# Optimization experiments

Measured on AMD Instinct MI355X. Metric: run time of the kernel, lower is better.

The kernel has to match this reference:

```python
import jax, jax.numpy as jnp
import numpy as np
import math

PRE_D = 2048   # pre_d_model (scaled from 8192)
D = 4096       # d_model (scaled from 16384)
N = 64         # d_state (scaled from 128)
K = 4          # d_conv
EXP = 2
L = 128        # sequence_length
DI1 = EXP * PRE_D
DI2 = EXP * D
DTR1 = math.ceil(PRE_D / 16)
DTR2 = math.ceil(D / 16)


def _sinusoid(max_len, d):
    pe = np.zeros((max_len, d), np.float32)
    pos = np.arange(max_len, dtype=np.float32)[:, None]
    div = np.exp(np.arange(0, d, 2, dtype=np.float32) * (-math.log(10000.0) / d))
    pe[:, 0::2] = np.sin(pos * div)
    pe[:, 1::2] = np.cos(pos * div)
    return jnp.asarray(pe)


def _mamba_params(key, d_in, d_out, di, dtr, n, k):
    ks = jax.random.split(key, 6)
    s = 0.02
    dt = jnp.exp(jax.random.uniform(ks[4], (di,)) * (math.log(0.1) - math.log(1e-3)) + math.log(1e-3))
    return dict(
        in_proj=jax.random.normal(ks[0], (2 * di, d_in)) * s,
        conv_w=jax.random.normal(ks[1], (di, k)) * s,
        conv_b=jnp.zeros((di,)),
        x_proj=jax.random.normal(ks[2], (dtr + 2 * n, di)) * s,
        dt_w=jax.random.normal(ks[3], (di, dtr)) * s,
        dt_b=jnp.log(jnp.expm1(dt)),  # softplus^-1 of dt init
        A_log=jnp.log(jnp.tile(jnp.arange(1, n + 1, dtype=jnp.float32), (di, 1))),
        D=jnp.ones((di,)),
        out_proj=jax.random.normal(ks[5], (d_out, di)) * s,
    )


def setup_inputs() -> dict:
    key = jax.random.key(0)
    k1, k2, k3, k4 = jax.random.split(key, 4)
    inp = {
        'pe': _sinusoid(L, PRE_D),                              # (L, PRE_D)
        'to_cond_w': jax.random.normal(k3, (PRE_D, 1)) * 0.02,  # Linear(1 -> PRE_D)
        'to_cond_b': jnp.zeros((PRE_D,)),
        'condition': jax.random.normal(k4, (1,)),
        'batch': 1,
    }
    for pref, p in (('m1_', _mamba_params(k1, PRE_D, PRE_D, DI1, DTR1, N, K)),
                    ('m2_', _mamba_params(k2, PRE_D, D, DI2, DTR2, N, K))):
        for name, v in p.items():
            inp[pref + name] = v
    return inp


def _silu(x):
    return x * jax.nn.sigmoid(x)


def _mamba(x, in_w, cw, cb, xp_w, dt_w, dt_b, A_log, Dp, out_w, dtr, n):
    # x: (B, L, d_in)
    xz = x @ in_w.T                     # (B, L, 2*di)
    xr, z = jnp.split(xz, 2, axis=-1)
    kk = cw.shape[1]
    Lx = xr.shape[1]
    xpad = jnp.pad(xr, ((0, 0), (kk - 1, 0), (0, 0)))  # causal pad
    conv = sum(cw[:, i] * xpad[:, i:i + Lx, :] for i in range(kk)) + cb
    xr = _silu(conv)
    dbc = xr @ xp_w.T                   # (B, L, dtr + 2n)
    dt = dbc[..., :dtr]
    Bm = dbc[..., dtr:dtr + n]
    Cm = dbc[..., dtr + n:]
    dt = jax.nn.softplus(dt @ dt_w.T + dt_b)           # (B, L, di)
    A = -jnp.exp(A_log)                                 # (di, n)
    dA = jnp.exp(jnp.einsum('bld,dn->bldn', dt, A))
    dBx = jnp.einsum('bld,bln,bld->bldn', dt, Bm, xr)

    def comb(c1, c2):
        a1, b1 = c1
        a2, b2 = c2
        return a2 * a1, a2 * b1 + b2

    _, h = jax.lax.associative_scan(comb, (dA, dBx), axis=1)  # (B, L, di, n)
    y = jnp.einsum('bldn,bln->bld', h, Cm) + xr * Dp
    y = y * _silu(z)
    return y @ out_w.T


def reference(pe, to_cond_w, to_cond_b, condition,
              m1_in_proj, m1_conv_w, m1_conv_b, m1_x_proj, m1_dt_w, m1_dt_b, m1_A_log, m1_D, m1_out_proj,
              m2_in_proj, m2_conv_w, m2_conv_b, m2_x_proj, m2_dt_w, m2_dt_b, m2_A_log, m2_D, m2_out_proj,
              batch):
    cond = condition.reshape(-1, 1, 1)
    c = jnp.einsum('bli,oi->blo', cond, to_cond_w) + to_cond_b   # (Bc,1,PRE_D)
    x = jnp.tile(pe[None], (batch, 1, 1)) + c                    # (B, L, PRE_D)
    x = _mamba(x, m1_in_proj, m1_conv_w, m1_conv_b, m1_x_proj, m1_dt_w, m1_dt_b,
               m1_A_log, m1_D, m1_out_proj, DTR1, N)
    x = _mamba(x, m2_in_proj, m2_conv_w, m2_conv_b, m2_x_proj, m2_dt_w, m2_dt_b,
               m2_A_log, m2_D, m2_out_proj, DTR2, N)
    return x
```

## Files before the change

### kernel.cpp

```cpp
#include <hip/hip_runtime.h>
#include <hip/hip_bf16.h>
#include <math.h>


typedef __attribute__((ext_vector_type(8))) short short8_t;
typedef __attribute__((ext_vector_type(4))) float f32x4;

__device__ __forceinline__ float sigmoidf_(float x) {
  return 1.0f / (1.0f + __expf(-x));
}
__device__ __forceinline__ float softplusf_(float x) {
  return fmaxf(x, 0.0f) + log1pf(expf(-fabsf(x)));
}
__device__ __forceinline__ void splitbf(float f, ushort& h, ushort& lo) {
  __hip_bfloat16 hb = __float2bfloat16(f);
  h = *reinterpret_cast<ushort*>(&hb);
  float hf = __bfloat162float(hb);
  __hip_bfloat16 lb = __float2bfloat16(f - hf);
  lo = *reinterpret_cast<ushort*>(&lb);
}
__device__ __forceinline__ size_t poff(int l, int d) {
  return (size_t)(d >> 5) * 8192 + (size_t)((d >> 3) & 3) * 1024 +
         (size_t)l * 8 + (d & 7);
}

__global__ __launch_bounds__(256) void k_prep(const float* __restrict__ pe,
                                              const float* __restrict__ cw,
                                              const float* __restrict__ cb,
                                              const float* __restrict__ cond,
                                              ushort* __restrict__ xp) {
  int i = blockIdx.x * 256 + threadIdx.x;
  int d = i & 2047;
  int l = i >> 11;
  float v = pe[i] + cond[0] * cw[d] + cb[d];
  ushort h, lo;
  splitbf(v, h, lo);
  size_t o = poff(l, d);
  xp[o] = h;
  xp[o + 4096] = lo;
}

#define KW 128
__global__ __launch_bounds__(256, 2) void k_gemmW(const ushort* __restrict__ Ap,
                                                  const float* __restrict__ W, int ldw,
                                                  float* __restrict__ P,
                                                  int N, int Ks) {
  __shared__ ushort Ws[2][2][16][66][8];

  const int n0   = blockIdx.x * 64;
  const int s    = blockIdx.z;
  const int kbeg = s * Ks;
  const int t    = threadIdx.x;
  const int l    = t & 63;
  const int w    = t >> 6;
  const int wm   = w >> 1;
  const int wn   = w & 1;
  const int lr   = l & 15;
  const int lg   = l >> 4;

  f32x4 acc[4][2];
#pragma unroll
  for (int mi = 0; mi < 4; ++mi)
#pragma unroll
    for (int ni = 0; ni < 2; ++ni) acc[mi][ni] = (f32x4)(0.0f);

  const int nIter = Ks / KW;
  const int j0    = (blockIdx.x * 3 + s) & (nIter - 1);

  const float* pWg = W + (size_t)(n0 + 16 * w) * ldw + kbeg + 2 * l;
  const int skb = l >> 2;
  const int se  = 2 * (l & 3);
  const ushort* pA0 = Ap + (size_t)(kbeg >> 5) * 8192;
  const int arow = 64 * wm + lr;
  const int brow = 32 * wn + lr;

#pragma unroll
  for (int i = 0; i < 16; ++i) {
    float2 v = *(const float2*)(pWg + (size_t)i * ldw + (size_t)j0 * KW);
    ushort h0, lo0, h1, lo1;
    splitbf(v.x, h0, lo0);
    splitbf(v.y, h1, lo1);
    ushort2 hh; hh.x = h0; hh.y = h1;
    ushort2 ll; ll.x = lo0; ll.y = lo1;
    *(ushort2*)&Ws[0][0][skb][16 * w + i][se] = hh;
    *(ushort2*)&Ws[0][1][skb][16 * w + i][se] = ll;
  }
  __syncthreads();

  for (int jj = 0; jj < nIter; ++jj) {
    const int cur = (j0 + jj) & (nIter - 1);
    const int bi  = jj & 1;
    const bool more = (jj + 1 < nIter);

    short8_t ah[4][4], al[4][4];
#pragma unroll
    for (int c = 0; c < 4; ++c) {
      const ushort* pAj = pA0 + (size_t)(cur * 4 + c) * 8192;
#pragma unroll
      for (int mi = 0; mi < 4; ++mi) {
        const size_t fo = (size_t)lg * 1024 + (size_t)(arow + 16 * mi) * 8;
        ah[c][mi] = *(const short8_t*)(pAj + fo);
        al[c][mi] = *(const short8_t*)(pAj + 4096 + fo);
      }
    }
    float2 wv[16];
    if (more) {
      const size_t ko = (size_t)((j0 + jj + 1) & (nIter - 1)) * KW;
#pragma unroll
      for (int i = 0; i < 16; ++i)
        wv[i] = *(const float2*)(pWg + (size_t)i * ldw + ko);
    }
#pragma unroll
    for (int c = 0; c < 4; ++c) {
      short8_t bh[2], bl[2];
#pragma unroll
      for (int ni = 0; ni < 2; ++ni) {
        bh[ni] = *(const short8_t*)&Ws[bi][0][c * 4 + lg][brow + 16 * ni][0];
        bl[ni] = *(const short8_t*)&Ws[bi][1][c * 4 + lg][brow + 16 * ni][0];
      }
#pragma unroll
      for (int mi = 0; mi < 4; ++mi)
#pragma unroll
        for (int ni = 0; ni < 2; ++ni) {
          acc[mi][ni] = __builtin_amdgcn_mfma_f32_16x16x32_bf16(ah[c][mi], bh[ni], acc[mi][ni], 0, 0, 0);
          acc[mi][ni] = __builtin_amdgcn_mfma_f32_16x16x32_bf16(al[c][mi], bh[ni], acc[mi][ni], 0, 0, 0);
          acc[mi][ni] = __builtin_amdgcn_mfma_f32_16x16x32_bf16(ah[c][mi], bl[ni], acc[mi][ni], 0, 0, 0);
        }
    }
    if (more) {
#pragma unroll
      for (int i = 0; i < 16; ++i) {
        ushort h0, lo0, h1, lo1;
        splitbf(wv[i].x, h0, lo0);
        splitbf(wv[i].y, h1, lo1);
        ushort2 hh; hh.x = h0; hh.y = h1;
        ushort2 ll; ll.x = lo0; ll.y = lo1;
        *(ushort2*)&Ws[bi ^ 1][0][skb][16 * w + i][se] = hh;
        *(ushort2*)&Ws[bi ^ 1][1][skb][16 * w + i][se] = ll;
      }
    }
    __syncthreads();
  }

  float* Pd = P + (size_t)s * 128 * N + n0 + 32 * wn;
#pragma unroll
  for (int mi = 0; mi < 4; ++mi)
#pragma unroll
    for (int ni = 0; ni < 2; ++ni) {
#pragma unroll
      for (int jj = 0; jj < 4; ++jj) {
        const int m = 64 * wm + 16 * mi + 4 * lg + jj;
        Pd[(size_t)m * N + 16 * ni + lr] = acc[mi][ni][jj];
      }
    }
}

#define KSTEP 32
__global__ __launch_bounds__(256, 2) void k_gemm(const ushort* __restrict__ Ap,
                                                 const float* __restrict__ W, int ldw,
                                                 float* __restrict__ P,
                                                 int N, int Ks) {
  __shared__ ushort Ws[2][2][4][128][8];

  const int n0   = blockIdx.x * 128;
  const int s    = blockIdx.z;
  const int kbeg = s * Ks;
  const int t    = threadIdx.x;
  const int l    = t & 63;
  const int w    = t >> 6;
  const int wm   = w >> 1;
  const int wn   = w & 1;
  const int lr   = l & 15;
  const int lg   = l >> 4;

  f32x4 acc[4][4];
#pragma unroll
  for (int mi = 0; mi < 4; ++mi)
#pragma unroll
    for (int ni = 0; ni < 4; ++ni) acc[mi][ni] = (f32x4)(0.0f);

  const int srow = t >> 3;
  const int sk16 = t & 7;
  const int skb  = sk16 >> 1;
  const int se0  = (sk16 & 1) * 4;
  const float* pWg = W + (size_t)(n0 + srow) * ldw + kbeg + sk16 * 4;

  const ushort* pAc = Ap + (size_t)(kbeg >> 5) * 8192;
  const int arow = 64 * wm + lr;
  const int brow = 64 * wn + lr;

  const int nIter = Ks / KSTEP;
  float4 wv[4];

#pragma unroll
  for (int r = 0; r < 4; ++r)
    wv[r] = *(const float4*)(pWg + (size_t)(r * 32) * ldw);
#pragma unroll
  for (int r = 0; r < 4; ++r) {
    ushort4 h4, l4;
    splitbf(wv[r].x, h4.x, l4.x); splitbf(wv[r].y, h4.y, l4.y);
    splitbf(wv[r].z, h4.z, l4.z); splitbf(wv[r].w, h4.w, l4.w);
    *(ushort4*)&Ws[0][0][skb][srow + 32 * r][se0] = h4;
    *(ushort4*)&Ws[0][1][skb][srow + 32 * r][se0] = l4;
  }
  __syncthreads();

  for (int j = 0; j < nIter; ++j) {
    const int bi = j & 1;
    const bool more = (j + 1 < nIter);

    const ushort* pAj = pAc + (size_t)j * 8192;
    short8_t ah[4], al[4];
#pragma unroll
    for (int mi = 0; mi < 4; ++mi) {
      const size_t fo = (size_t)lg * 1024 + (size_t)(arow + 16 * mi) * 8;
      ah[mi] = *(const short8_t*)(pAj + fo);
      al[mi] = *(const short8_t*)(pAj + 4096 + fo);
    }
    if (more) {
      const size_t ko = (size_t)(j + 1) * KSTEP;
#pragma unroll
      for (int r = 0; r < 4; ++r)
        wv[r] = *(const float4*)(pWg + ko + (size_t)(r * 32) * ldw);
    }
    short8_t bh[4], bl[4];
#pragma unroll
    for (int ni = 0; ni < 4; ++ni) {
      bh[ni] = *(const short8_t*)&Ws[bi][0][lg][brow + 16 * ni][0];
      bl[ni] = *(const short8_t*)&Ws[bi][1][lg][brow + 16 * ni][0];
    }
#pragma unroll
    for (int mi = 0; mi < 4; ++mi)
#pragma unroll
      for (int ni = 0; ni < 4; ++ni) {
        acc[mi][ni] = __builtin_amdgcn_mfma_f32_16x16x32_bf16(ah[mi], bh[ni], acc[mi][ni], 0, 0, 0);
        acc[mi][ni] = __builtin_amdgcn_mfma_f32_16x16x32_bf16(al[mi], bh[ni], acc[mi][ni], 0, 0, 0);
        acc[mi][ni] = __builtin_amdgcn_mfma_f32_16x16x32_bf16(ah[mi], bl[ni], acc[mi][ni], 0, 0, 0);
      }
    if (more) {
#pragma unroll
      for (int r = 0; r < 4; ++r) {
        ushort4 h4, l4;
        splitbf(wv[r].x, h4.x, l4.x); splitbf(wv[r].y, h4.y, l4.y);
        splitbf(wv[r].z, h4.z, l4.z); splitbf(wv[r].w, h4.w, l4.w);
        *(ushort4*)&Ws[bi ^ 1][0][skb][srow + 32 * r][se0] = h4;
        *(ushort4*)&Ws[bi ^ 1][1][skb][srow + 32 * r][se0] = l4;
      }
    }
    __syncthreads();
  }

  float* Pd = P + (size_t)s * 128 * N + n0 + 64 * wn;
#pragma unroll
  for (int mi = 0; mi < 4; ++mi)
#pragma unroll
    for (int ni = 0; ni < 4; ++ni) {
#pragma unroll
      for (int jj = 0; jj < 4; ++jj) {
        const int m = 64 * wm + 16 * mi + 4 * lg + jj;
        Pd[(size_t)m * N + 16 * ni + lr] = acc[mi][ni][jj];
      }
    }
}

__global__ __launch_bounds__(256) void k_reduce(const float* __restrict__ P,
                                                float* __restrict__ Y,
                                                ushort* __restrict__ Yp,
                                                int MN, int N, int S, int ep,
                                                const float* __restrict__ bias) {
  int i = (blockIdx.x * 256 + threadIdx.x) * 4;
  if (i >= MN) return;
  float4 v = *(const float4*)&P[i];
  for (int s = 1; s < S; ++s) {
    float4 p = *(const float4*)&P[(size_t)s * MN + i];
    v.x += p.x; v.y += p.y; v.z += p.z; v.w += p.w;
  }
  int n = i % N;
  int l = i / N;
  if (ep & 1) {
    const float4 b = *(const float4*)&bias[n];
    v.x = softplusf_(v.x + b.x);
    v.y = softplusf_(v.y + b.y);
    v.z = softplusf_(v.z + b.z);
    v.w = softplusf_(v.w + b.w);
  }
  if (ep & 4) *(float4*)&Y[i] = v;
  if (ep & 2) {
    ushort4 h4, l4;
    splitbf(v.x, h4.x, l4.x);
    splitbf(v.y, h4.y, l4.y);
    splitbf(v.z, h4.z, l4.z);
    splitbf(v.w, h4.w, l4.w);
    size_t o = poff(l, n);
    *(ushort4*)&Yp[o] = h4;
    *(ushort4*)&Yp[o + 4096] = l4;
  }
}

__global__ __launch_bounds__(256) void k_reduceA(const float* __restrict__ P,
                                                 float* __restrict__ Y, int MN) {
  int g = blockIdx.y;
  int i = (blockIdx.x * 256 + threadIdx.x) * 4;
  if (i >= MN) return;
  const float* Pp = P + (size_t)g * 8 * MN;
  float4 v = *(const float4*)&Pp[i];
  for (int s = 1; s < 8; ++s) {
    float4 p = *(const float4*)&Pp[(size_t)s * MN + i];
    v.x += p.x; v.y += p.y; v.z += p.z; v.w += p.w;
  }
  *(float4*)&Y[(size_t)g * MN + i] = v;
}

__global__ __launch_bounds__(256) void k_conv_silu(const float* __restrict__ xz,
                                                   const float* __restrict__ cw,
                                                   const float* __restrict__ cb,
                                                   float* __restrict__ xc,
                                                   ushort* __restrict__ xcp,
                                                   int DI, int lg2DI) {
  int i = blockIdx.x * 256 + threadIdx.x;
  int l = i >> lg2DI;
  int d = i & (DI - 1);
  const float4 w = *(const float4*)&cw[d * 4];
  const float* xr = xz + d;
  int ld = 2 * DI;
  float s = cb[d];
  s += w.w * xr[l * ld];
  if (l >= 1) s += w.z * xr[(l - 1) * ld];
  if (l >= 2) s += w.y * xr[(l - 2) * ld];
  if (l >= 3) s += w.x * xr[(l - 3) * ld];
  float v = s * sigmoidf_(s);
  xc[i] = v;
  ushort h, lo;
  splitbf(v, h, lo);
  size_t o = poff(l, d);
  xcp[o] = h;
  xcp[o + 4096] = lo;
}

__global__ __launch_bounds__(256) void k_scan(const float* __restrict__ dt,
                                              const float* __restrict__ xc,
                                              const float* __restrict__ dbc,
                                              const float* __restrict__ A_log,
                                              const float* __restrict__ Dp,
                                              float* __restrict__ y,
                                              int DI, int DTR) {
  __shared__ float cs[4][32][65];
  const int wid = threadIdx.x >> 6;
  const int n   = threadIdx.x & 63;
  const int d   = blockIdx.x * 4 + wid;
  const int du  = __builtin_amdgcn_readfirstlane(d);
  const float A  = -__expf(A_log[(size_t)du * 64 + n]);
  const float Dd = Dp[du];
  const int ldbc = DTR + 128;
  const float* Bp = dbc + DTR + n;
  const float* Cp = dbc + DTR + 64 + n;
  float h = 0.0f;
  for (int l0 = 0; l0 < 128; l0 += 32) {
#pragma unroll 8
    for (int l = l0; l < l0 + 32; ++l) {
      float dtv = dt[(size_t)l * DI + du];
      float xcv = xc[(size_t)l * DI + du];
      float dA  = __expf(dtv * A);
      float bx  = dtv * xcv;
      h = fmaf(dA, h, bx * Bp[(size_t)l * ldbc]);
      cs[wid][l - l0][n] = h * Cp[(size_t)l * ldbc];
    }
    __syncthreads();
    const int r = n & 31, hf = n >> 5;
    float ssum = 0.0f;
#pragma unroll
    for (int j = 0; j < 32; ++j) ssum += cs[wid][r][hf * 32 + j];
    ssum += __shfl_xor(ssum, 32, 64);
    if (n < 32) {
      int ll = l0 + r;
      float xcv = xc[(size_t)ll * DI + du];
      y[(size_t)ll * DI + du] = ssum + xcv * Dd;
    }
    __syncthreads();
  }
}

__global__ __launch_bounds__(256) void k_gate(const float* __restrict__ yb,
                                              const float* __restrict__ xz,
                                              ushort* __restrict__ yp,
                                              int DI, int lg2DI) {
  int i = blockIdx.x * 256 + threadIdx.x;
  int l = i >> lg2DI;
  int d = i & (DI - 1);
  float z = xz[((size_t)l << (lg2DI + 1)) + DI + d];
  float v = yb[i] * (z * sigmoidf_(z));
  ushort h, lo;
  splitbf(v, h, lo);
  size_t o = poff(l, d);
  yp[o] = h;
  yp[o + 4096] = lo;
}

struct GemmCtx {
  float* part;
  float* part2;
  long long cap;
};

static inline void reduce_stage(float* dstF, ushort* dstP, int N, int S, int ep,
                                const float* bias, const GemmCtx& cx,
                                hipStream_t stream) {
  const int MN = 128 * N;
  const int rb = (MN / 4 + 255) / 256;
  if (S <= 16) {
    k_reduce<<<rb, 256, 0, stream>>>(cx.part, dstF, dstP, MN, N, S, ep, bias);
  } else {
    k_reduceA<<<dim3(rb, S / 8), 256, 0, stream>>>(cx.part, cx.part2, MN);
    k_reduce<<<rb, 256, 0, stream>>>(cx.part2, dstF, dstP, MN, N, S / 8, ep, bias);
  }
}

static inline void gemmS(const ushort* Ap, const float* W, int ldw,
                         float* dstF, ushort* dstP,
                         int N, int K, int Sdes, int ep,
                         const float* bias, const GemmCtx& cx, hipStream_t stream) {
  int S = Sdes;
  if (S > K / KSTEP) S = K / KSTEP;
  if (S < 1) S = 1;
  while (S > 1 && (long long)S * 128 * N > cx.cap) S >>= 1;
  const int Ks = K / S;
  const bool direct = (S == 1 && ep == 4);
  dim3 g(N / 128, 1, S);
  k_gemm<<<g, 256, 0, stream>>>(Ap, W, ldw, direct ? dstF : cx.part, N, Ks);
  if (!direct) reduce_stage(dstF, dstP, N, S, ep, bias, cx, stream);
}

static inline void gemmW(const ushort* Ap, const float* W, int ldw,
                         float* dstF, ushort* dstP,
                         int N, int K, int Sdes, int ep,
                         const float* bias, const GemmCtx& cx, hipStream_t stream) {
  int S = Sdes;
  if (S > K / KW) S = K / KW;
  if (S < 1) S = 1;
  while (S > 1 && (long long)S * 128 * N > cx.cap) S >>= 1;
  const int Ks = K / S;
  const bool direct = (S == 1 && ep == 4);
  dim3 g(N / 64, 1, S);
  k_gemmW<<<g, 256, 0, stream>>>(Ap, W, ldw, direct ? dstF : cx.part, N, Ks);
  if (!direct) reduce_stage(dstF, dstP, N, S, ep, bias, cx, stream);
}

extern "C" void kernel_launch(void* const* d_in, const int* in_sizes, int n_in,
                              void* d_out, int out_size, void* d_ws, size_t ws_size,
                              hipStream_t stream) {
  const float* pe        = (const float*)d_in[0];
  const float* to_cond_w = (const float*)d_in[1];
  const float* to_cond_b = (const float*)d_in[2];
  const float* condition = (const float*)d_in[3];
  const int o = (in_sizes[4] == 1) ? 5 : 4;
  const float* m1_in_proj  = (const float*)d_in[o + 0];
  const float* m1_conv_w   = (const float*)d_in[o + 1];
  const float* m1_conv_b   = (const float*)d_in[o + 2];
  const float* m1_x_proj   = (const float*)d_in[o + 3];
  const float* m1_dt_w     = (const float*)d_in[o + 4];
  const float* m1_dt_b     = (const float*)d_in[o + 5];
  const float* m1_A_log    = (const float*)d_in[o + 6];
  const float* m1_D        = (const float*)d_in[o + 7];
  const float* m1_out_proj = (const float*)d_in[o + 8];
  const float* m2_in_proj  = (const float*)d_in[o + 9];
  const float* m2_conv_w   = (const float*)d_in[o + 10];
  const float* m2_conv_b   = (const float*)d_in[o + 11];
  const float* m2_x_proj   = (const float*)d_in[o + 12];
  const float* m2_dt_w     = (const float*)d_in[o + 13];
  const float* m2_dt_b     = (const float*)d_in[o + 14];
  const float* m2_A_log    = (const float*)d_in[o + 15];
  const float* m2_D        = (const float*)d_in[o + 16];
  const float* m2_out_proj = (const float*)d_in[o + 17];

  float* ws = (float*)d_ws;
  float*  xz   = ws;
  float*  xc   = ws + 2097152;
  float*  dbc  = ws + 3145728;
  float*  dtb  = ws + 3194880;
  float*  yb   = ws + 4243456;
  ushort* x0p  = (ushort*)(ws + 5292032);
  ushort* xcp  = (ushort*)(ws + 5554176);
  ushort* dbcp = (ushort*)(ws + 6602752);
  ushort* ybp  = (ushort*)(ws + 6651904);
  ushort* midp = (ushort*)(ws + 7700480);
  float*  part2 = ws + 7962624;
  float*  part  = ws + 8749056;

  GemmCtx cx;
  cx.part = part;
  cx.part2 = part2;
  cx.cap = (long long)(ws_size / 4) - 8749056;
  if (cx.cap < 0) cx.cap = 0;

  k_prep<<<1024, 256, 0, stream>>>(pe, to_cond_w, to_cond_b, condition, x0p);

  gemmW(x0p, m1_in_proj, 2048, xz, nullptr, 8192, 2048, 4, 4, nullptr, cx, stream);
  k_conv_silu<<<(128 * 4096) / 256, 256, 0, stream>>>(xz, m1_conv_w, m1_conv_b,
                                                      xc, xcp, 4096, 12);
  gemmS(xcp, m1_x_proj, 4096, dbc, dbcp, 256, 4096, 128, 6, nullptr, cx, stream);
  gemmS(dbcp, m1_dt_w, 128, dtb, nullptr, 4096, 128, 4, 5, m1_dt_b, cx, stream);
  k_scan<<<1024, 256, 0, stream>>>(dtb, xc, dbc, m1_A_log, m1_D, yb, 4096, 128);
  k_gate<<<(128 * 4096) / 256, 256, 0, stream>>>(yb, xz, ybp, 4096, 12);
  gemmW(ybp, m1_out_proj, 4096, nullptr, midp, 2048, 4096, 16, 2, nullptr, cx, stream);

  gemmW(midp, m2_in_proj, 2048, xz, nullptr, 16384, 2048, 2, 4, nullptr, cx, stream);
  k_conv_silu<<<(128 * 8192) / 256, 256, 0, stream>>>(xz, m2_conv_w, m2_conv_b,
                                                      xc, xcp, 8192, 13);
  gemmS(xcp, m2_x_proj, 8192, dbc, dbcp, 384, 8192, 128, 6, nullptr, cx, stream);
  gemmS(dbcp, m2_dt_w, 256, dtb, nullptr, 8192, 256, 4, 5, m2_dt_b, cx, stream);
  k_scan<<<2048, 256, 0, stream>>>(dtb, xc, dbc, m2_A_log, m2_D, yb, 8192, 256);
  k_gate<<<(128 * 8192) / 256, 256, 0, stream>>>(yb, xz, ybp, 8192, 13);
  gemmW(ybp, m2_out_proj, 8192, (float*)d_out, nullptr, 4096, 8192, 8, 4, nullptr, cx, stream);
}
```

Baseline: 378.2 us.

## Stream fp32 weights into LDS via global_load_lds and split to bf16 at use

The weight GEMM kernel now copies raw fp32 weight tiles straight into XOR-swizzled LDS with the direct global-to-LDS load builtin, double-buffered over 32-wide K steps. The hi/lo bf16 split happens after the LDS read, using a cheaper truncation-based split instead of round-to-nearest conversions. The N tile doubles to 128 per block, and the split-K factors double to keep the grid populated. This removes register staging and the convert-then-store step on the load path, but repeats the split work per warp, holds more accumulators, and the truncated hi/lo split changes rounding slightly.

```diff
diff --git a/kernel.cpp b/kernel.cpp
--- a/kernel.cpp
+++ b/kernel.cpp
@@ -19,9 +19,20 @@
   __hip_bfloat16 lb = __float2bfloat16(f - hf);
   lo = *reinterpret_cast<ushort*>(&lb);
 }
+__device__ __forceinline__ void tsplit(float f, ushort& h, ushort& lo) {
+  unsigned u = __float_as_uint(f);
+  h = (ushort)(u >> 16);
+  float r = f - __uint_as_float(u & 0xFFFF0000u);
+  lo = (ushort)(__float_as_uint(r) >> 16);
+}
 __device__ __forceinline__ size_t poff(int l, int d) {
   return (size_t)(d >> 5) * 8192 + (size_t)((d >> 3) & 3) * 1024 +
          (size_t)l * 8 + (d & 7);
+}
+__device__ __forceinline__ void g2l16(const float* g, float* lp) {
+  __builtin_amdgcn_global_load_lds(
+      (const __attribute__((address_space(1))) unsigned int*)g,
+      (__attribute__((address_space(3))) unsigned int*)lp, 16, 0, 0);
 }
 
 __global__ __launch_bounds__(256) void k_prep(const float* __restrict__ pe,
@@ -40,14 +51,14 @@
   xp[o + 4096] = lo;
 }
 
-#define KW 128
-__global__ __launch_bounds__(256, 2) void k_gemmW(const ushort* __restrict__ Ap,
+#define KWS 32
+__global__ __launch_bounds__(256, 3) void k_gemmW(const ushort* __restrict__ Ap,
                                                   const float* __restrict__ W, int ldw,
                                                   float* __restrict__ P,
                                                   int N, int Ks) {
-  __shared__ ushort Ws[2][2][16][66][8];
-
-  const int n0   = blockIdx.x * 64;
+  __shared__ float Wlds[2][128][32];
+
+  const int n0   = blockIdx.x * 128;
   const int s    = blockIdx.z;
   const int kbeg = s * Ks;
   const int t    = threadIdx.x;
@@ -58,95 +69,79 @@
   const int lr   = l & 15;
   const int lg   = l >> 4;
 
-  f32x4 acc[4][2];
+  f32x4 acc[4][4];
 #pragma unroll
   for (int mi = 0; mi < 4; ++mi)
 #pragma unroll
-    for (int ni = 0; ni < 2; ++ni) acc[mi][ni] = (f32x4)(0.0f);
-
-  const int nIter = Ks / KW;
-  const int j0    = (blockIdx.x * 3 + s) & (nIter - 1);
-
-  const float* pWg = W + (size_t)(n0 + 16 * w) * ldw + kbeg + 2 * l;
-  const int skb = l >> 2;
-  const int se  = 2 * (l & 3);
+    for (int ni = 0; ni < 4; ++ni) acc[mi][ni] = (f32x4)(0.0f);
+
+  const int grow = l >> 3;
+  const int gg   = (l & 7) ^ (grow & 7);
+  const float* gW[4];
+#pragma unroll
+  for (int i = 0; i < 4; ++i)
+    gW[i] = W + (size_t)(n0 + 8 * (w * 4 + i) + grow) * ldw + kbeg + gg * 4;
+
   const ushort* pA0 = Ap + (size_t)(kbeg >> 5) * 8192;
   const int arow = 64 * wm + lr;
-  const int brow = 32 * wn + lr;
-
-#pragma unroll
-  for (int i = 0; i < 16; ++i) {
-    float2 v = *(const float2*)(pWg + (size_t)i * ldw + (size_t)j0 * KW);
-    ushort h0, lo0, h1, lo1;
-    splitbf(v.x, h0, lo0);
-    splitbf(v.y, h1, lo1);
-    ushort2 hh; hh.x = h0; hh.y = h1;
-    ushort2 ll; ll.x = lo0; ll.y = lo1;
-    *(ushort2*)&Ws[0][0][skb][16 * w + i][se] = hh;
-    *(ushort2*)&Ws[0][1][skb][16 * w + i][se] = ll;
-  }
+  const int rsw  = lr & 7;
+
+  const int nIter = Ks / KWS;
+
+#pragma unroll
+  for (int i = 0; i < 4; ++i)
+    g2l16(gW[i], &Wlds[0][0][0] + (w * 4 + i) * 256);
   __syncthreads();
 
-  for (int jj = 0; jj < nIter; ++jj) {
-    const int cur = (j0 + jj) & (nIter - 1);
-    const int bi  = jj & 1;
-    const bool more = (jj + 1 < nIter);
-
-    short8_t ah[4][4], al[4][4];
-#pragma unroll
-    for (int c = 0; c < 4; ++c) {
-      const ushort* pAj = pA0 + (size_t)(cur * 4 + c) * 8192;
+  for (int j = 0; j < nIter; ++j) {
+    const int bi = j & 1;
+
+    const ushort* pAj = pA0 + (size_t)j * 8192;
+    short8_t ah[4], al[4];
+#pragma unroll
+    for (int mi = 0; mi < 4; ++mi) {
+      const size_t fo = (size_t)lg * 1024 + (size_t)(arow + 16 * mi) * 8;
+      ah[mi] = *(const short8_t*)(pAj + fo);
+      al[mi] = *(const short8_t*)(pAj + 4096 + fo);
+    }
+    if (j + 1 < nIter) {
+#pragma unroll
+      for (int i = 0; i < 4; ++i)
+        g2l16(gW[i] + (size_t)(j + 1) * KWS,
+              &Wlds[bi ^ 1][0][0] + (w * 4 + i) * 256);
+    }
+    const float* Wb = &Wlds[bi][0][0];
+#pragma unroll
+    for (int ni = 0; ni < 4; ++ni) {
+      const int r = 64 * wn + 16 * ni + lr;
+      const float4 v0 = *(const float4*)(Wb + r * 32 + (((2 * lg) ^ rsw) * 4));
+      const float4 v1 = *(const float4*)(Wb + r * 32 + (((2 * lg + 1) ^ rsw) * 4));
+      short8_t bh, bl;
+      {
+        const float f8[8] = {v0.x, v0.y, v0.z, v0.w, v1.x, v1.y, v1.z, v1.w};
+#pragma unroll
+        for (int e = 0; e < 8; ++e) {
+          ushort h, lo;
+          tsplit(f8[e], h, lo);
+          bh[e] = (short)h;
+          bl[e] = (short)lo;
+        }
+      }
 #pragma unroll
       for (int mi = 0; mi < 4; ++mi) {
-        const size_t fo = (size_t)lg * 1024 + (size_t)(arow + 16 * mi) * 8;
-        ah[c][mi] = *(const short8_t*)(pAj + fo);
-        al[c][mi] = *(const short8_t*)(pAj + 4096 + fo);
+        acc[mi][ni] = __builtin_amdgcn_mfma_f32_16x16x32_bf16(ah[mi], bh, acc[mi][ni], 0, 0, 0);
+        acc[mi][ni] = __builtin_amdgcn_mfma_f32_16x16x32_bf16(al[mi], bh, acc[mi][ni], 0, 0, 0);
+        acc[mi][ni] = __builtin_amdgcn_mfma_f32_16x16x32_bf16(ah[mi], bl, acc[mi][ni], 0, 0, 0);
       }
     }
-    float2 wv[16];
-    if (more) {
-      const size_t ko = (size_t)((j0 + jj + 1) & (nIter - 1)) * KW;
-#pragma unroll
-      for (int i = 0; i < 16; ++i)
-        wv[i] = *(const float2*)(pWg + (size_t)i * ldw + ko);
-    }
-#pragma unroll
-    for (int c = 0; c < 4; ++c) {
-      short8_t bh[2], bl[2];
-#pragma unroll
-      for (int ni = 0; ni < 2; ++ni) {
-        bh[ni] = *(const short8_t*)&Ws[bi][0][c * 4 + lg][brow + 16 * ni][0];
-        bl[ni] = *(const short8_t*)&Ws[bi][1][c * 4 + lg][brow + 16 * ni][0];
-      }
-#pragma unroll
-      for (int mi = 0; mi < 4; ++mi)
-#pragma unroll
-        for (int ni = 0; ni < 2; ++ni) {
-          acc[mi][ni] = __builtin_amdgcn_mfma_f32_16x16x32_bf16(ah[c][mi], bh[ni], acc[mi][ni], 0, 0, 0);
-          acc[mi][ni] = __builtin_amdgcn_mfma_f32_16x16x32_bf16(al[c][mi], bh[ni], acc[mi][ni], 0, 0, 0);
-          acc[mi][ni] = __builtin_amdgcn_mfma_f32_16x16x32_bf16(ah[c][mi], bl[ni], acc[mi][ni], 0, 0, 0);
-        }
-    }
-    if (more) {
-#pragma unroll
-      for (int i = 0; i < 16; ++i) {
-        ushort h0, lo0, h1, lo1;
-        splitbf(wv[i].x, h0, lo0);
-        splitbf(wv[i].y, h1, lo1);
-        ushort2 hh; hh.x = h0; hh.y = h1;
-        ushort2 ll; ll.x = lo0; ll.y = lo1;
-        *(ushort2*)&Ws[bi ^ 1][0][skb][16 * w + i][se] = hh;
-        *(ushort2*)&Ws[bi ^ 1][1][skb][16 * w + i][se] = ll;
-      }
-    }
     __syncthreads();
   }
 
-  float* Pd = P + (size_t)s * 128 * N + n0 + 32 * wn;
+  float* Pd = P + (size_t)s * 128 * N + n0 + 64 * wn;
 #pragma unroll
   for (int mi = 0; mi < 4; ++mi)
 #pragma unroll
-    for (int ni = 0; ni < 2; ++ni) {
+    for (int ni = 0; ni < 4; ++ni) {
 #pragma unroll
       for (int jj = 0; jj < 4; ++jj) {
         const int m = 64 * wm + 16 * mi + 4 * lg + jj;
@@ -435,12 +430,12 @@
                          int N, int K, int Sdes, int ep,
                          const float* bias, const GemmCtx& cx, hipStream_t stream) {
   int S = Sdes;
-  if (S > K / KW) S = K / KW;
+  if (S > K / KWS) S = K / KWS;
   if (S < 1) S = 1;
   while (S > 1 && (long long)S * 128 * N > cx.cap) S >>= 1;
   const int Ks = K / S;
   const bool direct = (S == 1 && ep == 4);
-  dim3 g(N / 64, 1, S);
+  dim3 g(N / 128, 1, S);
   k_gemmW<<<g, 256, 0, stream>>>(Ap, W, ldw, direct ? dstF : cx.part, N, Ks);
   if (!direct) reduce_stage(dstF, dstP, N, S, ep, bias, cx, stream);
 }
@@ -494,21 +489,21 @@
 
   k_prep<<<1024, 256, 0, stream>>>(pe, to_cond_w, to_cond_b, condition, x0p);
 
-  gemmW(x0p, m1_in_proj, 2048, xz, nullptr, 8192, 2048, 4, 4, nullptr, cx, stream);
+  gemmW(x0p, m1_in_proj, 2048, xz, nullptr, 8192, 2048, 8, 4, nullptr, cx, stream);
   k_conv_silu<<<(128 * 4096) / 256, 256, 0, stream>>>(xz, m1_conv_w, m1_conv_b,
                                                       xc, xcp, 4096, 12);
   gemmS(xcp, m1_x_proj, 4096, dbc, dbcp, 256, 4096, 128, 6, nullptr, cx, stream);
   gemmS(dbcp, m1_dt_w, 128, dtb, nullptr, 4096, 128, 4, 5, m1_dt_b, cx, stream);
   k_scan<<<1024, 256, 0, stream>>>(dtb, xc, dbc, m1_A_log, m1_D, yb, 4096, 128);
   k_gate<<<(128 * 4096) / 256, 256, 0, stream>>>(yb, xz, ybp, 4096, 12);
-  gemmW(ybp, m1_out_proj, 4096, nullptr, midp, 2048, 4096, 16, 2, nullptr, cx, stream);
-
-  gemmW(midp, m2_in_proj, 2048, xz, nullptr, 16384, 2048, 2, 4, nullptr, cx, stream);
+  gemmW(ybp, m1_out_proj, 4096, nullptr, midp, 2048, 4096, 32, 2, nullptr, cx, stream);
+
+  gemmW(midp, m2_in_proj, 2048, xz, nullptr, 16384, 2048, 4, 4, nullptr, cx, stream);
   k_conv_silu<<<(128 * 8192) / 256, 256, 0, stream>>>(xz, m2_conv_w, m2_conv_b,
                                                       xc, xcp, 8192, 13);
   gemmS(xcp, m2_x_proj, 8192, dbc, dbcp, 384, 8192, 128, 6, nullptr, cx, stream);
   gemmS(dbcp, m2_dt_w, 256, dtb, nullptr, 8192, 256, 4, 5, m2_dt_b, cx, stream);
   k_scan<<<2048, 256, 0, stream>>>(dtb, xc, dbc, m2_A_log, m2_D, yb, 8192, 256);
   k_gate<<<(128 * 8192) / 256, 256, 0, stream>>>(yb, xz, ybp, 8192, 13);
-  gemmW(ybp, m2_out_proj, 8192, (float*)d_out, nullptr, 4096, 8192, 8, 4, nullptr, cx, stream);
-}
+  gemmW(ybp, m2_out_proj, 8192, (float*)d_out, nullptr, 4096, 8192, 16, 4, nullptr, cx, stream);
+}
```

Measured after the change: 352.4 us. 6.8% less time.
